# Kernel tuning notes

Measured on AMD Instinct MI355X. Metric: run time of the kernel, lower is better.

## Reference

```python
import jax, jax.numpy as jnp
import numpy as np

NUM_HEADS = 16


def setup_inputs() -> dict:
    key = jax.random.key(0)
    k1, k2, k3 = jax.random.split(key, 3)
    B, S, D = 2, 2048, 1024
    x = jax.random.normal(k1, (B, S, D), dtype=jnp.float32)
    # qkv_bias=False -> no bias on qkv projection; output Dense has default bias
    w_qkv = jax.random.normal(k2, (D, 3 * D), dtype=jnp.float32) * (1.0 / np.sqrt(D))
    w_out = jax.random.normal(k3, (D, D), dtype=jnp.float32) * (1.0 / np.sqrt(D))
    b_out = jnp.zeros((D,), dtype=jnp.float32)
    return {"x": x, "w_qkv": w_qkv, "w_out": w_out, "b_out": b_out}


def reference(x, w_qkv, w_out, b_out):
    B, S, D = x.shape
    H = NUM_HEADS
    Dh = D // H
    scale = 1.0 / np.sqrt(Dh).astype(np.float32)

    qkv = jnp.einsum('bsd,de->bse', x, w_qkv)           # [B,S,3D]
    q, k, v = jnp.split(qkv, 3, axis=-1)
    split = lambda t: t.reshape(B, S, H, Dh).transpose(0, 2, 1, 3)  # [B,H,S,Dh]
    q, k, v = split(q), split(k), split(v)

    attn = jnp.einsum('bhid,bhjd->bhij', q, k) * scale  # [B,H,S,S]
    # mask=None -> all-ones mask combined with causal mask => causal float mask
    causal = jnp.tril(jnp.ones((S, S), dtype=jnp.float32))[None, None]
    attn = causal * attn + (1.0 - causal) * (-1e9)
    attn = jax.nn.softmax(attn, axis=-1)

    out = jnp.einsum('bhij,bhjd->bhid', attn, v)        # [B,H,S,Dh]
    out = out.transpose(0, 2, 1, 3).reshape(B, S, D)    # merge heads
    return jnp.einsum('bsd,de->bse', out, w_out) + b_out
```

## Files before the change

kernel.cpp:

```cpp
#include <hip/hip_runtime.h>

typedef unsigned short u16;
typedef __bf16 bf16x8 __attribute__((ext_vector_type(8)));
typedef unsigned short u16x8 __attribute__((ext_vector_type(8)));
typedef float f32x4 __attribute__((ext_vector_type(4)));

union Frag { u16x8 u; bf16x8 b; };

__device__ __forceinline__ u16 f2bf(float f) {
  unsigned u = __builtin_bit_cast(unsigned, f);
  u += 0x7fff + ((u >> 16) & 1);
  return (u16)(u >> 16);
}

__device__ __forceinline__ f32x4 mfma16(bf16x8 a, bf16x8 b, f32x4 c) {
  return __builtin_amdgcn_mfma_f32_16x16x32_bf16(a, b, c, 0, 0, 0);
}

__device__ __forceinline__ float exp2_raw(float x) {
  float r;
  asm("v_exp_f32 %0, %1" : "=v"(r) : "v"(x));
  return r;
}

typedef const __attribute__((address_space(1))) void* as1cv;
typedef __attribute__((address_space(3))) void* as3v;

__device__ __forceinline__ void glds16(const u16* g, u16* l) {
  __builtin_amdgcn_global_load_lds((as1cv)g, (as3v)l, 16, 0, 0);
}

__global__ __launch_bounds__(256) void castf_bf(const float* __restrict__ src,
                                                u16* __restrict__ dst, int n4) {
  int i = blockIdx.x * blockDim.x + threadIdx.x;
  int stride = gridDim.x * blockDim.x;
  for (; i < n4; i += stride) {
    float4 v = ((const float4*)src)[i];
    ushort4 o;
    o.x = f2bf(v.x); o.y = f2bf(v.y); o.z = f2bf(v.z); o.w = f2bf(v.w);
    ((ushort4*)dst)[i] = o;
  }
}

__global__ __launch_bounds__(256) void cast_transpose(const float* __restrict__ src,
                                                      u16* __restrict__ dst, int K, int N) {
  __shared__ float tile[32][33];
  int tn = N >> 5;
  int bk = blockIdx.x / tn, bn = blockIdx.x % tn;
  int k0 = bk << 5, n0 = bn << 5;
  int tx = threadIdx.x, ty = threadIdx.y;
#pragma unroll
  for (int i = 0; i < 4; i++)
    tile[ty + 8 * i][tx] = src[(size_t)(k0 + ty + 8 * i) * N + n0 + tx];
  __syncthreads();
#pragma unroll
  for (int i = 0; i < 4; i++)
    dst[(size_t)(n0 + ty + 8 * i) * K + k0 + tx] = f2bf(tile[tx][ty + 8 * i]);
}

template <int FP32OUT>
__global__ __launch_bounds__(256) void gemm_bt(const u16* __restrict__ A,
                                               const u16* __restrict__ BT,
                                               void* __restrict__ Cout,
                                               const float* __restrict__ bias,
                                               int N, int K, int nbc) {
  __shared__ u16 Al[2][128 * 32];
  __shared__ u16 Bl[2][128 * 32];
  int bid = blockIdx.x;
  int br = bid / nbc, bc = bid % nbc;
  int tid = threadIdx.x;
  int w = tid >> 6, l = tid & 63;
  int lg = l >> 4, lq = l & 15;
  int wr = w >> 1, wc = w & 1;

  f32x4 acc[4][4];
#pragma unroll
  for (int m = 0; m < 4; m++)
#pragma unroll
    for (int n = 0; n < 4; n++)
      acc[m][n] = (f32x4){0.f, 0.f, 0.f, 0.f};

  const u16* Ab = A + (size_t)(br * 128 + 32 * w + (l >> 2)) * K + (l & 3) * 8;
  const u16* Bb = BT + (size_t)(bc * 128 + 32 * w + (l >> 2)) * K + (l & 3) * 8;

  auto stage = [&](int it, int buf) {
    int kt = it * 32;
    u16* ald = &Al[buf][32 * w * 32];
    u16* bld = &Bl[buf][32 * w * 32];
    glds16(Ab + kt, ald);
    glds16(Ab + (size_t)16 * K + kt, ald + 16 * 32);
    glds16(Bb + kt, bld);
    glds16(Bb + (size_t)16 * K + kt, bld + 16 * 32);
  };

  int nk = K >> 5;
  stage(0, 0);
  __syncthreads();

  for (int it = 0; it < nk; ++it) {
    int buf = it & 1;
    if (it + 1 < nk) stage(it + 1, buf ^ 1);

    Frag af[4], bf[4];
#pragma unroll
    for (int m = 0; m < 4; m++)
      af[m].u = *(const u16x8*)(&Al[buf][(64 * wr + 16 * m + lq) * 32 + lg * 8]);
#pragma unroll
    for (int n = 0; n < 4; n++)
      bf[n].u = *(const u16x8*)(&Bl[buf][(64 * wc + 16 * n + lq) * 32 + lg * 8]);
    __builtin_amdgcn_s_setprio(1);
#pragma unroll
    for (int m = 0; m < 4; m++)
#pragma unroll
      for (int n = 0; n < 4; n++)
        acc[m][n] = mfma16(af[m].b, bf[n].b, acc[m][n]);
    __builtin_amdgcn_s_setprio(0);
    __syncthreads();
  }

  int row0 = br * 128 + 64 * wr + lg * 4;
  int col0 = bc * 128 + 64 * wc + lq;
  if (FP32OUT) {
    float* C = (float*)Cout;
#pragma unroll
    for (int n = 0; n < 4; n++) {
      float bv = bias[col0 + 16 * n];
#pragma unroll
      for (int m = 0; m < 4; m++)
#pragma unroll
        for (int r = 0; r < 4; r++)
          C[(size_t)(row0 + 16 * m + r) * N + col0 + 16 * n] = acc[m][n][r] + bv;
    }
  } else {
    u16* C = (u16*)Cout;
#pragma unroll
    for (int n = 0; n < 4; n++)
#pragma unroll
      for (int m = 0; m < 4; m++)
#pragma unroll
        for (int r = 0; r < 4; r++)
          C[(size_t)(row0 + 16 * m + r) * N + col0 + 16 * n] = f2bf(acc[m][n][r]);
  }
}

__global__ __launch_bounds__(256) void build_vt(const u16* __restrict__ qkv,
                                                u16* __restrict__ vt) {
  __shared__ u16 t[64][65];
  int bid = blockIdx.x;
  int s0 = (bid & 31) * 64;
  int bh = bid >> 5;
  int b = bh >> 4, h = bh & 15;
  int tid = threadIdx.x;
  int r = tid >> 2, c4 = (tid & 3) * 16;
  const u16* srow = qkv + (size_t)(b * 2048 + s0 + r) * 3072 + 2048 + h * 64 + c4;
  u16x8 v0 = *(const u16x8*)(srow);
  u16x8 v1 = *(const u16x8*)(srow + 8);
#pragma unroll
  for (int j = 0; j < 8; j++) { t[r][c4 + j] = v0[j]; t[r][c4 + 8 + j] = v1[j]; }
  __syncthreads();
  int dh = tid >> 2, sc = (tid & 3) * 16;
  u16 outv[16];
#pragma unroll
  for (int i = 0; i < 16; ++i) {
    int e = sc + i;
    int b32 = e >> 5, e32 = e & 31;
    int k = ((e32 >> 2) & 1) * 16 + (e32 >> 3) * 4 + (e32 & 3);
    outv[i] = t[b32 * 32 + k][dh];
  }
  u16* drow = vt + ((size_t)bh * 64 + dh) * 2048 + s0 + sc;
  *(u16x8*)drow = *(u16x8*)&outv[0];
  *(u16x8*)(drow + 8) = *(u16x8*)&outv[8];
}

__global__ __launch_bounds__(256) void flash_attn(const u16* __restrict__ qkv,
                                                  const u16* __restrict__ vt,
                                                  u16* __restrict__ aout) {
  __shared__ __align__(16) u16 pool[2][8192];
  const float SL2E = 0.18033688011112043f;
  int bid = blockIdx.x;
  int bh = bid & 31;
  int qb = 31 - (bid >> 5);
  int b = bh >> 4, h = bh & 15;
  int tid = threadIdx.x;
  int w = tid >> 6, l = tid & 63;
  int lg = l >> 4, lq = l & 15;
  int q0w = qb * 64 + w * 16;
  int qidx = q0w + lq;
  int ntiles = qb + 1;

  const size_t rs = 3072;
  int srw = l >> 3;
  int scol = 8 * ((l & 7) ^ srw);
  const u16* kg = qkv + (size_t)(b * 2048) * rs + 1024 + h * 64;
  const u16* vg = vt + (size_t)bh * 64 * 2048;
  int r0 = (w * 2 + 0) * 8 + srw;
  int r1 = (w * 2 + 1) * 8 + srw;
  int swz = (lq & 7) << 3;

  Frag qf0, qf1;
  const u16* qbase = qkv + (size_t)(b * 2048 + q0w + lq) * rs + h * 64 + lg * 8;
  qf0.u = *(const u16x8*)(qbase);
  qf1.u = *(const u16x8*)(qbase + 32);

  float lam = 0.f;
  f32x4 o[4];
#pragma unroll
  for (int d = 0; d < 4; ++d) o[d] = (f32x4){0.f, 0.f, 0.f, 0.f};

  auto stage = [&](int tile, int buf) {
    int kt2 = tile * 64;
    u16* nb = &pool[buf][0];
    glds16(kg + (size_t)(kt2 + r0) * rs + scol, nb + (w * 2 + 0) * 512);
    glds16(kg + (size_t)(kt2 + r1) * rs + scol, nb + (w * 2 + 1) * 512);
    glds16(vg + (size_t)r0 * 2048 + kt2 + scol, nb + 4096 + (w * 2 + 0) * 512);
    glds16(vg + (size_t)r1 * 2048 + kt2 + scol, nb + 4096 + (w * 2 + 1) * 512);
  };

  stage(0, 0);
  __syncthreads();

  for (int t = 0; t < ntiles; ++t) {
    if (t + 1 < ntiles) stage(t + 1, (t + 1) & 1);
    const u16* Kl = &pool[t & 1][0];
    const u16* Vl = &pool[t & 1][4096];
    int kt = t * 64;

    f32x4 s[4];
    __builtin_amdgcn_s_setprio(1);
#pragma unroll
    for (int sub = 0; sub < 4; ++sub) {
      int row = sub * 16 + lq;
      Frag k0, k1;
      k0.u = *(const u16x8*)(Kl + row * 64 + ((lg * 8) ^ swz));
      k1.u = *(const u16x8*)(Kl + row * 64 + ((32 + lg * 8) ^ swz));
      f32x4 z = {0.f, 0.f, 0.f, 0.f};
      s[sub] = mfma16(k0.b, qf0.b, z);
      s[sub] = mfma16(k1.b, qf1.b, s[sub]);
    }
    __builtin_amdgcn_s_setprio(0);

    if (t == qb) {
#pragma unroll
      for (int sub = 0; sub < 4; ++sub)
#pragma unroll
        for (int r = 0; r < 4; ++r) {
          int key = kt + sub * 16 + lg * 4 + r;
          if (key > qidx) s[sub][r] = -1e30f;
        }
    }

    Frag pf[2];
#pragma unroll
    for (int hf = 0; hf < 2; ++hf)
#pragma unroll
      for (int r = 0; r < 4; ++r) {
        float p0 = exp2_raw(s[2 * hf][r] * SL2E);
        float p1 = exp2_raw(s[2 * hf + 1][r] * SL2E);
        lam += p0 + p1;
        pf[hf].b[r] = (__bf16)p0;
        pf[hf].b[4 + r] = (__bf16)p1;
      }

    __builtin_amdgcn_s_setprio(1);
#pragma unroll
    for (int d = 0; d < 4; ++d) {
      int row = d * 16 + lq;
      Frag vf0, vf1;
      vf0.u = *(const u16x8*)(Vl + row * 64 + ((lg * 8) ^ swz));
      vf1.u = *(const u16x8*)(Vl + row * 64 + ((32 + lg * 8) ^ swz));
      o[d] = mfma16(vf0.b, pf[0].b, o[d]);
      o[d] = mfma16(vf1.b, pf[1].b, o[d]);
    }
    __builtin_amdgcn_s_setprio(0);
    __syncthreads();
  }

  lam += __shfl_xor(lam, 16);
  lam += __shfl_xor(lam, 32);
  float inv = 1.0f / lam;

  u16* Ost = &pool[0][0] + w * (16 * 72);
#pragma unroll
  for (int d = 0; d < 4; ++d)
#pragma unroll
    for (int r = 0; r < 4; ++r)
      Ost[lq * 72 + d * 16 + lg * 4 + r] = f2bf(o[d][r] * inv);
  int q = l >> 2, c16 = (l & 3) * 16;
  u16x8 t0, t1;
#pragma unroll
  for (int j = 0; j < 8; j++) { t0[j] = Ost[q * 72 + c16 + j]; t1[j] = Ost[q * 72 + c16 + 8 + j]; }
  u16* orow = aout + (size_t)(b * 2048 + qb * 64 + w * 16 + q) * 1024 + h * 64 + c16;
  *(u16x8*)orow = t0;
  *(u16x8*)(orow + 8) = t1;
}

extern "C" void kernel_launch(void* const* d_in, const int* in_sizes, int n_in,
                              void* d_out, int out_size, void* d_ws, size_t ws_size,
                              hipStream_t stream) {
  const float* x    = (const float*)d_in[0];
  const float* wqkv = (const float*)d_in[1];
  const float* wout = (const float*)d_in[2];
  const float* bout = (const float*)d_in[3];
  float* out = (float*)d_out;

  char* ws = (char*)d_ws;
  u16* xb    = (u16*)(ws);
  u16* wqkvT = (u16*)(ws + 8388608);
  u16* woutT = (u16*)(ws + 14680064);
  u16* qkvb  = (u16*)(ws + 16777216);
  u16* vtb   = (u16*)(ws + 41943040);
  u16* aoutb = (u16*)(ws + 50331648);

  castf_bf<<<1024, 256, 0, stream>>>(x, xb, (4096 * 1024) / 4);
  cast_transpose<<<(1024 / 32) * (3072 / 32), dim3(32, 8), 0, stream>>>(wqkv, wqkvT, 1024, 3072);
  cast_transpose<<<(1024 / 32) * (1024 / 32), dim3(32, 8), 0, stream>>>(wout, woutT, 1024, 1024);

  gemm_bt<0><<<(4096 / 128) * (3072 / 128), 256, 0, stream>>>(xb, wqkvT, qkvb, nullptr,
                                                              3072, 1024, 3072 / 128);
  build_vt<<<1024, 256, 0, stream>>>(qkvb, vtb);
  flash_attn<<<1024, 256, 0, stream>>>(qkvb, vtb, aoutb);

  gemm_bt<1><<<(4096 / 128) * (1024 / 128), 256, 0, stream>>>(aoutb, woutT, out, bout,
                                                              1024, 1024, 1024 / 128);
}
```

Measured before the change: 113.9 us.

## Replace QKV projection GEMM with 256x256-tile, 8-wave pipelined kernel

Adds a new bf16 GEMM kernel with 256x256 output tiles, 512 threads, a 64-wide K step, XOR-swizzled LDS, and double-buffered global-to-LDS loads interleaved per quadrant with explicit waitcnt and barriers. It also remaps block IDs in groups of eight to improve L2 locality, and uses it for the QKV projection. The goal is more data reuse per loaded tile and better overlap of loads with MFMA work. In exchange it launches only 192 workgroups, which may underfill the GPU, and it needs more LDS and registers per block.

```diff
diff --git a/kernel.cpp b/kernel.cpp
--- a/kernel.cpp
+++ b/kernel.cpp
@@ -29,6 +29,8 @@
 __device__ __forceinline__ void glds16(const u16* g, u16* l) {
   __builtin_amdgcn_global_load_lds((as1cv)g, (as3v)l, 16, 0, 0);
 }
+
+#define FENCE asm volatile("" ::: "memory")
 
 __global__ __launch_bounds__(256) void castf_bf(const float* __restrict__ src,
                                                 u16* __restrict__ dst, int n4) {
@@ -56,6 +58,119 @@
 #pragma unroll
   for (int i = 0; i < 4; i++)
     dst[(size_t)(n0 + ty + 8 * i) * K + k0 + tx] = f2bf(tile[tx][ty + 8 * i]);
+}
+
+__global__ __launch_bounds__(512) void gemm256(const u16* __restrict__ A,
+                                               const u16* __restrict__ BT,
+                                               u16* __restrict__ C,
+                                               int M, int N, int K, int nbc) {
+  __shared__ __align__(16) u16 lds[2][4][8192];
+  int nwg = gridDim.x;
+  int cpx = nwg >> 3;
+  int bid = blockIdx.x;
+  int swz = (bid & 7) * cpx + (bid >> 3);
+  int br = swz / nbc, bc = swz % nbc;
+
+  int tid = threadIdx.x;
+  int w = tid >> 6, l = tid & 63;
+  int lg = l >> 4, lq = l & 15;
+  int wr = w >> 2, wc = w & 3;
+
+  int rr = tid >> 3;
+  int gl = (tid & 7) ^ (rr & 7);
+  const u16* Abase = A + (size_t)(br * 256) * K + gl * 8;
+  const u16* Bbase = BT + (size_t)(bc * 256) * K + gl * 8;
+
+  f32x4 acc[2][2][4][2];
+#pragma unroll
+  for (int i = 0; i < 2; ++i)
+#pragma unroll
+    for (int j = 0; j < 2; ++j)
+#pragma unroll
+      for (int m = 0; m < 4; ++m)
+#pragma unroll
+        for (int n = 0; n < 2; ++n)
+          acc[i][j][m][n] = (f32x4){0.f, 0.f, 0.f, 0.f};
+
+  auto stage = [&](int tile, int buf, int hh) {
+    int kt = tile << 6;
+    const u16* s0;
+    if (hh == 0)      s0 = Abase + (size_t)rr * K + kt;
+    else if (hh == 1) s0 = Bbase + (size_t)rr * K + kt;
+    else if (hh == 2) s0 = Bbase + (size_t)(128 + rr) * K + kt;
+    else              s0 = Abase + (size_t)(128 + rr) * K + kt;
+    u16* d = &lds[buf][hh][w * 512];
+    glds16(s0, d);
+    glds16(s0 + (size_t)64 * K, d + 4096);
+  };
+
+  int NT = K >> 6;
+  stage(0, 0, 0); stage(0, 0, 1); stage(0, 0, 2); stage(0, 0, 3);
+  asm volatile("s_waitcnt vmcnt(4)" ::: "memory");
+  FENCE; __builtin_amdgcn_s_barrier(); __builtin_amdgcn_sched_barrier(0);
+
+  for (int t = 0; t < NT; ++t) {
+    int buf = t & 1;
+    int hn = (t + 1 < NT);
+#pragma unroll
+    for (int q = 0; q < 4; ++q) {
+      const int mh = q >> 1, nh = q & 1;
+      const u16* Ar = &lds[buf][mh ? 3 : 0][0];
+      const u16* Br = &lds[buf][1 + nh][0];
+      Frag a[4][2], bb[2][2];
+#pragma unroll
+      for (int m = 0; m < 4; ++m) {
+        int ar = wr * 64 + m * 16 + lq;
+#pragma unroll
+        for (int kk = 0; kk < 2; ++kk)
+          a[m][kk].u = *(const u16x8*)(Ar + ar * 64 + (((kk * 4 + lg) ^ (ar & 7)) << 3));
+      }
+#pragma unroll
+      for (int n = 0; n < 2; ++n) {
+        int brr = wc * 32 + n * 16 + lq;
+#pragma unroll
+        for (int kk = 0; kk < 2; ++kk)
+          bb[n][kk].u = *(const u16x8*)(Br + brr * 64 + (((kk * 4 + lg) ^ (brr & 7)) << 3));
+      }
+      if (hn) stage(t + 1, buf ^ 1, q);
+      FENCE; __builtin_amdgcn_s_barrier(); __builtin_amdgcn_sched_barrier(0);
+      __builtin_amdgcn_s_setprio(1);
+#pragma unroll
+      for (int m = 0; m < 4; ++m)
+#pragma unroll
+        for (int n = 0; n < 2; ++n) {
+          acc[mh][nh][m][n] = mfma16(a[m][0].b, bb[n][0].b, acc[mh][nh][m][n]);
+          acc[mh][nh][m][n] = mfma16(a[m][1].b, bb[n][1].b, acc[mh][nh][m][n]);
+        }
+      __builtin_amdgcn_s_setprio(0);
+      if (q == 0) {
+        if (hn) asm volatile("s_waitcnt vmcnt(4)" ::: "memory");
+        else    asm volatile("s_waitcnt vmcnt(2)" ::: "memory");
+      } else if (q == 1) {
+        if (hn) asm volatile("s_waitcnt vmcnt(4)" ::: "memory");
+        else    asm volatile("s_waitcnt vmcnt(0)" ::: "memory");
+      } else if (q == 3) {
+        if (hn) asm volatile("s_waitcnt vmcnt(4)" ::: "memory");
+      }
+      FENCE; __builtin_amdgcn_s_barrier(); __builtin_amdgcn_sched_barrier(0);
+    }
+  }
+
+#pragma unroll
+  for (int mh = 0; mh < 2; ++mh)
+#pragma unroll
+    for (int m = 0; m < 4; ++m) {
+      int row0 = br * 256 + mh * 128 + wr * 64 + m * 16 + lg * 4;
+#pragma unroll
+      for (int nh = 0; nh < 2; ++nh)
+#pragma unroll
+        for (int n = 0; n < 2; ++n) {
+          int col = bc * 256 + nh * 128 + wc * 32 + n * 16 + lq;
+#pragma unroll
+          for (int r = 0; r < 4; ++r)
+            C[(size_t)(row0 + r) * N + col] = f2bf(acc[mh][nh][m][n][r]);
+        }
+    }
 }
 
 template <int FP32OUT>
@@ -315,8 +430,8 @@
   cast_transpose<<<(1024 / 32) * (3072 / 32), dim3(32, 8), 0, stream>>>(wqkv, wqkvT, 1024, 3072);
   cast_transpose<<<(1024 / 32) * (1024 / 32), dim3(32, 8), 0, stream>>>(wout, woutT, 1024, 1024);
 
-  gemm_bt<0><<<(4096 / 128) * (3072 / 128), 256, 0, stream>>>(xb, wqkvT, qkvb, nullptr,
-                                                              3072, 1024, 3072 / 128);
+  gemm256<<<(4096 / 256) * (3072 / 256), 512, 0, stream>>>(xb, wqkvT, qkvb,
+                                                           4096, 3072, 1024, 3072 / 256);
   build_vt<<<1024, 256, 0, stream>>>(qkvb, vtb);
   flash_attn<<<1024, 256, 0, stream>>>(qkvb, vtb, aoutb);
 
```

Result: slower. 117.2 us (+2.9%).

## Fuse V-transpose into QKV GEMM epilogue, merge weight casts, swizzle GEMM blocks

Applied to the files above, without the earlier changes.

The QKV GEMM epilogue now writes V tiles straight into the permuted transposed layout that flash attention expects, so the separate build_vt kernel and its extra read and write of V go away. The two weight cast-transpose launches become one kernel that picks its source by block index. Both GEMMs remap block IDs with an XCD-style swizzle to improve L2 locality. The V epilogue now does scattered 8-byte stores, and the index permutation has to match the old build_vt mapping exactly.

```diff
diff --git a/kernel.cpp b/kernel.cpp
--- a/kernel.cpp
+++ b/kernel.cpp
@@ -42,11 +42,18 @@
   }
 }
 
-__global__ __launch_bounds__(256) void cast_transpose(const float* __restrict__ src,
-                                                      u16* __restrict__ dst, int K, int N) {
+__global__ __launch_bounds__(256) void cast_transpose2(const float* __restrict__ s1,
+                                                       u16* __restrict__ d1,
+                                                       const float* __restrict__ s2,
+                                                       u16* __restrict__ d2) {
   __shared__ float tile[32][33];
+  int bid = blockIdx.x;
+  const float* src; u16* dst; int N;
+  if (bid < 3072) { src = s1; dst = d1; N = 3072; }
+  else            { bid -= 3072; src = s2; dst = d2; N = 1024; }
+  const int K = 1024;
   int tn = N >> 5;
-  int bk = blockIdx.x / tn, bn = blockIdx.x % tn;
+  int bk = bid / tn, bn = bid % tn;
   int k0 = bk << 5, n0 = bn << 5;
   int tx = threadIdx.x, ty = threadIdx.y;
 #pragma unroll
@@ -58,16 +65,17 @@
     dst[(size_t)(n0 + ty + 8 * i) * K + k0 + tx] = f2bf(tile[tx][ty + 8 * i]);
 }
 
-template <int FP32OUT>
-__global__ __launch_bounds__(256) void gemm_bt(const u16* __restrict__ A,
-                                               const u16* __restrict__ BT,
-                                               void* __restrict__ Cout,
-                                               const float* __restrict__ bias,
-                                               int N, int K, int nbc) {
+__global__ __launch_bounds__(256) void gemm_qkv(const u16* __restrict__ A,
+                                                const u16* __restrict__ BT,
+                                                u16* __restrict__ C,
+                                                u16* __restrict__ vt,
+                                                int N, int K, int nbc) {
   __shared__ u16 Al[2][128 * 32];
   __shared__ u16 Bl[2][128 * 32];
+  int nwg = gridDim.x;
   int bid = blockIdx.x;
-  int br = bid / nbc, bc = bid % nbc;
+  int swz = (bid & 7) * (nwg >> 3) + (bid >> 3);
+  int br = swz / nbc, bc = swz % nbc;
   int tid = threadIdx.x;
   int w = tid >> 6, l = tid & 63;
   int lg = l >> 4, lq = l & 15;
@@ -120,19 +128,7 @@
 
   int row0 = br * 128 + 64 * wr + lg * 4;
   int col0 = bc * 128 + 64 * wc + lq;
-  if (FP32OUT) {
-    float* C = (float*)Cout;
-#pragma unroll
-    for (int n = 0; n < 4; n++) {
-      float bv = bias[col0 + 16 * n];
-#pragma unroll
-      for (int m = 0; m < 4; m++)
-#pragma unroll
-        for (int r = 0; r < 4; r++)
-          C[(size_t)(row0 + 16 * m + r) * N + col0 + 16 * n] = acc[m][n][r] + bv;
-    }
-  } else {
-    u16* C = (u16*)Cout;
+  if (bc < 16) {
 #pragma unroll
     for (int n = 0; n < 4; n++)
 #pragma unroll
@@ -140,36 +136,98 @@
 #pragma unroll
         for (int r = 0; r < 4; r++)
           C[(size_t)(row0 + 16 * m + r) * N + col0 + 16 * n] = f2bf(acc[m][n][r]);
-  }
-}
-
-__global__ __launch_bounds__(256) void build_vt(const u16* __restrict__ qkv,
-                                                u16* __restrict__ vt) {
-  __shared__ u16 t[64][65];
+  } else {
+#pragma unroll
+    for (int n = 0; n < 4; n++) {
+      int vcol = col0 + 16 * n - 2048;
+      int h = vcol >> 6, dh = vcol & 63;
+#pragma unroll
+      for (int m = 0; m < 4; m++) {
+        int s_abs = row0 + 16 * m;
+        int bb = s_abs >> 11;
+        int s = s_abs & 2047;
+        int e = (s >> 5) * 32 + ((s >> 4) & 1) * 4 + ((s >> 2) & 3) * 8;
+        ushort4 v;
+        v.x = f2bf(acc[m][n][0]); v.y = f2bf(acc[m][n][1]);
+        v.z = f2bf(acc[m][n][2]); v.w = f2bf(acc[m][n][3]);
+        *(ushort4*)&vt[((size_t)(bb * 16 + h) * 64 + dh) * 2048 + e] = v;
+      }
+    }
+  }
+}
+
+__global__ __launch_bounds__(256) void gemm_bt(const u16* __restrict__ A,
+                                               const u16* __restrict__ BT,
+                                               float* __restrict__ Cout,
+                                               const float* __restrict__ bias,
+                                               int N, int K, int nbc) {
+  __shared__ u16 Al[2][128 * 32];
+  __shared__ u16 Bl[2][128 * 32];
+  int nwg = gridDim.x;
   int bid = blockIdx.x;
-  int s0 = (bid & 31) * 64;
-  int bh = bid >> 5;
-  int b = bh >> 4, h = bh & 15;
+  int swz = (bid & 7) * (nwg >> 3) + (bid >> 3);
+  int br = swz / nbc, bc = swz % nbc;
   int tid = threadIdx.x;
-  int r = tid >> 2, c4 = (tid & 3) * 16;
-  const u16* srow = qkv + (size_t)(b * 2048 + s0 + r) * 3072 + 2048 + h * 64 + c4;
-  u16x8 v0 = *(const u16x8*)(srow);
-  u16x8 v1 = *(const u16x8*)(srow + 8);
-#pragma unroll
-  for (int j = 0; j < 8; j++) { t[r][c4 + j] = v0[j]; t[r][c4 + 8 + j] = v1[j]; }
+  int w = tid >> 6, l = tid & 63;
+  int lg = l >> 4, lq = l & 15;
+  int wr = w >> 1, wc = w & 1;
+
+  f32x4 acc[4][4];
+#pragma unroll
+  for (int m = 0; m < 4; m++)
+#pragma unroll
+    for (int n = 0; n < 4; n++)
+      acc[m][n] = (f32x4){0.f, 0.f, 0.f, 0.f};
+
+  const u16* Ab = A + (size_t)(br * 128 + 32 * w + (l >> 2)) * K + (l & 3) * 8;
+  const u16* Bb = BT + (size_t)(bc * 128 + 32 * w + (l >> 2)) * K + (l & 3) * 8;
+
+  auto stage = [&](int it, int buf) {
+    int kt = it * 32;
+    u16* ald = &Al[buf][32 * w * 32];
+    u16* bld = &Bl[buf][32 * w * 32];
+    glds16(Ab + kt, ald);
+    glds16(Ab + (size_t)16 * K + kt, ald + 16 * 32);
+    glds16(Bb + kt, bld);
+    glds16(Bb + (size_t)16 * K + kt, bld + 16 * 32);
+  };
+
+  int nk = K >> 5;
+  stage(0, 0);
   __syncthreads();
-  int dh = tid >> 2, sc = (tid & 3) * 16;
-  u16 outv[16];
-#pragma unroll
-  for (int i = 0; i < 16; ++i) {
-    int e = sc + i;
-    int b32 = e >> 5, e32 = e & 31;
-    int k = ((e32 >> 2) & 1) * 16 + (e32 >> 3) * 4 + (e32 & 3);
-    outv[i] = t[b32 * 32 + k][dh];
-  }
-  u16* drow = vt + ((size_t)bh * 64 + dh) * 2048 + s0 + sc;
-  *(u16x8*)drow = *(u16x8*)&outv[0];
-  *(u16x8*)(drow + 8) = *(u16x8*)&outv[8];
+
+  for (int it = 0; it < nk; ++it) {
+    int buf = it & 1;
+    if (it + 1 < nk) stage(it + 1, buf ^ 1);
+
+    Frag af[4], bf[4];
+#pragma unroll
+    for (int m = 0; m < 4; m++)
+      af[m].u = *(const u16x8*)(&Al[buf][(64 * wr + 16 * m + lq) * 32 + lg * 8]);
+#pragma unroll
+    for (int n = 0; n < 4; n++)
+      bf[n].u = *(const u16x8*)(&Bl[buf][(64 * wc + 16 * n + lq) * 32 + lg * 8]);
+    __builtin_amdgcn_s_setprio(1);
+#pragma unroll
+    for (int m = 0; m < 4; m++)
+#pragma unroll
+      for (int n = 0; n < 4; n++)
+        acc[m][n] = mfma16(af[m].b, bf[n].b, acc[m][n]);
+    __builtin_amdgcn_s_setprio(0);
+    __syncthreads();
+  }
+
+  int row0 = br * 128 + 64 * wr + lg * 4;
+  int col0 = bc * 128 + 64 * wc + lq;
+#pragma unroll
+  for (int n = 0; n < 4; n++) {
+    float bv = bias[col0 + 16 * n];
+#pragma unroll
+    for (int m = 0; m < 4; m++)
+#pragma unroll
+      for (int r = 0; r < 4; r++)
+        Cout[(size_t)(row0 + 16 * m + r) * N + col0 + 16 * n] = acc[m][n][r] + bv;
+  }
 }
 
 __global__ __launch_bounds__(256) void flash_attn(const u16* __restrict__ qkv,
@@ -312,14 +370,12 @@
   u16* aoutb = (u16*)(ws + 50331648);
 
   castf_bf<<<1024, 256, 0, stream>>>(x, xb, (4096 * 1024) / 4);
-  cast_transpose<<<(1024 / 32) * (3072 / 32), dim3(32, 8), 0, stream>>>(wqkv, wqkvT, 1024, 3072);
-  cast_transpose<<<(1024 / 32) * (1024 / 32), dim3(32, 8), 0, stream>>>(wout, woutT, 1024, 1024);
-
-  gemm_bt<0><<<(4096 / 128) * (3072 / 128), 256, 0, stream>>>(xb, wqkvT, qkvb, nullptr,
-                                                              3072, 1024, 3072 / 128);
-  build_vt<<<1024, 256, 0, stream>>>(qkvb, vtb);
+  cast_transpose2<<<3072 + 1024, dim3(32, 8), 0, stream>>>(wqkv, wqkvT, wout, woutT);
+
+  gemm_qkv<<<(4096 / 128) * (3072 / 128), 256, 0, stream>>>(xb, wqkvT, qkvb, vtb,
+                                                            3072, 1024, 3072 / 128);
   flash_attn<<<1024, 256, 0, stream>>>(qkvb, vtb, aoutb);
 
-  gemm_bt<1><<<(4096 / 128) * (1024 / 128), 256, 0, stream>>>(aoutb, woutT, out, bout,
-                                                              1024, 1024, 1024 / 128);
-}
+  gemm_bt<<<(4096 / 128) * (1024 / 128), 256, 0, stream>>>(aoutb, woutT, out, bout,
+                                                           1024, 1024, 1024 / 128);
+}
```

After: 106.0 us. -6.9%, faster.
